# Kernel optimization log

Measured on AMD Instinct MI355X. Metric: run time of the kernel, lower is better.

The kernel has to match this reference:

```python
import jax, jax.numpy as jnp
import numpy as np


def setup_inputs() -> dict:
    key = jax.random.key(0)
    ks = jax.random.split(key, 8)
    B, L, F, H, A = 128, 196, 2048, 512, 512
    features = jax.random.normal(ks[0], (B, L, F), dtype=jnp.float32)
    hidden_state = jax.random.normal(ks[1], (B, H), dtype=jnp.float32)
    # Linear params (PyTorch layout: weight [out, in], bias [out]); scaled like kaiming-uniform
    W_enc = jax.random.normal(ks[2], (A, F), dtype=jnp.float32) / np.sqrt(F)
    b_enc = jnp.zeros((A,), dtype=jnp.float32)
    W_dec = jax.random.normal(ks[3], (A, H), dtype=jnp.float32) / np.sqrt(H)
    b_dec = jnp.zeros((A,), dtype=jnp.float32)
    W_com = jax.random.normal(ks[4], (1, A), dtype=jnp.float32) / np.sqrt(A)
    b_com = jnp.zeros((1,), dtype=jnp.float32)
    return {
        "features": features, "hidden_state": hidden_state,
        "W_enc": W_enc, "b_enc": b_enc,
        "W_dec": W_dec, "b_dec": b_dec,
        "W_com": W_com, "b_com": b_com,
    }


def reference(features, hidden_state, W_enc, b_enc, W_dec, b_dec, W_com, b_com):
    # encoder_context: [B, L, A]
    enc = jnp.einsum('blf,af->bla', features, W_enc) + b_enc
    # decoder_context: [B, 1, A]
    dec = (hidden_state @ W_dec.T + b_dec)[:, None, :]
    # relu + linear to scalar score (dropout in eval mode = identity): [B, L]
    scores = jnp.einsum('bla,a->bl', jax.nn.relu(enc + dec), W_com[0]) + b_com[0]
    alpha = jax.nn.softmax(scores, axis=1)  # [B, L]
    weighted_features = jnp.einsum('blf,bl->bf', features, alpha)  # [B, F]
    return weighted_features, alpha
```

## Files before the change

### kernel.cpp

```cpp
#include <hip/hip_runtime.h>
#include <hip/hip_bf16.h>
#include <math.h>

#define B_  128
#define L_  196
#define F_  2048
#define H_  512
#define A_  512
#define ML_ (B_*L_)

typedef _Float16 half8 __attribute__((ext_vector_type(8)));
typedef _Float16 half4v __attribute__((ext_vector_type(4)));
typedef float f32x4 __attribute__((ext_vector_type(4)));

__device__ __forceinline__ void gld_lds16(const void* g, void* l) {
  __builtin_amdgcn_global_load_lds((const __attribute__((address_space(1))) void*)g,
                                   (__attribute__((address_space(3))) void*)l, 16, 0, 0);
}

__global__ __launch_bounds__(256) void k_prep(const float4* __restrict__ Wenc4,
                                              half4v* __restrict__ wH,
                                              const float* __restrict__ hs,
                                              const float* __restrict__ Wdec,
                                              const float* __restrict__ bdec,
                                              const float* __restrict__ benc,
                                              float* __restrict__ dec,
                                              float* __restrict__ scores) {
  const int b = blockIdx.x, t = threadIdx.x;

  {
    const int base = b * 2048 + t;
    float4 v[8];
#pragma unroll
    for (int j = 0; j < 8; j++) v[j] = Wenc4[base + j * 256];
#pragma unroll
    for (int j = 0; j < 8; j++) {
      half4v o = { (_Float16)v[j].x, (_Float16)v[j].y, (_Float16)v[j].z, (_Float16)v[j].w };
      wH[base + j * 256] = o;
    }
  }

  const int g = b * 256 + t;
  if (g < ML_) scores[g] = 0.f;

  __shared__ float h[H_];
  h[t]       = hs[b * H_ + t];
  h[t + 256] = hs[b * H_ + t + 256];
  __syncthreads();

#pragma unroll
  for (int r = 0; r < 2; r++) {
    const int a = t + r * 256;
    float acc = bdec[a] + benc[a];
    const float4* wr = (const float4*)(Wdec + (size_t)a * H_);
#pragma unroll 4
    for (int k4 = 0; k4 < H_ / 4; k4++) {
      const float4 w = wr[k4];
      acc += w.x * h[4*k4] + w.y * h[4*k4+1] + w.z * h[4*k4+2] + w.w * h[4*k4+3];
    }
    dec[b * A_ + a] = acc;
  }
}

__global__ __launch_bounds__(256) void k_scores_mfma(const float* __restrict__ fA,
                                                     const _Float16* __restrict__ fB,
                                                     const float* __restrict__ dec,
                                                     const float* __restrict__ wcom,
                                                     float* __restrict__ scores) {
  __shared__ float     As[128 * 64];
  __shared__ _Float16  Bs[128 * 64];
  __shared__ float decS[2][128];

  const int tid  = threadIdx.x;
  const int lane = tid & 63;
  const int w    = tid >> 6;
  const int a0   = blockIdx.x * 128;
  const int m0   = blockIdx.y * 128;
  const int wm   = w & 1;
  const int wn   = w >> 1;
  const int quad = lane >> 4;
  const int l16  = lane & 15;

  f32x4 acc[4][4];
#pragma unroll
  for (int i = 0; i < 4; i++)
#pragma unroll
    for (int j = 0; j < 4; j++)
#pragma unroll
      for (int k = 0; k < 4; k++) acc[i][j][k] = 0.f;

  const int b0 = m0 / L_;
  {
    const int i = tid >> 7;
    const int j = tid & 127;
    int bb = b0 + i; if (bb > B_ - 1) bb = B_ - 1;
    decS[i][j] = dec[bb * A_ + a0 + j];
  }

  const int srow4  = lane >> 4;
  const int slot16 = lane & 15;
  const float* pA[8];
#pragma unroll
  for (int i = 0; i < 8; i++) {
    const int rb = w * 32 + i * 4;
    const int r  = rb + srow4;
    const int ch = slot16 ^ (r & 15);
    pA[i] = fA + (size_t)(m0 + r) * F_ + ch * 4;
  }
  const int srow8 = lane >> 3;
  const int slot8 = lane & 7;
  const _Float16* pB[4];
#pragma unroll
  for (int i = 0; i < 4; i++) {
    const int rb = w * 32 + i * 8;
    const int r  = rb + srow8;
    const int ch = slot8 ^ (r & 7);
    pB[i] = fB + (size_t)(a0 + r) * F_ + ch * 8;
  }

  for (int kt = 0; kt < F_; kt += 64) {
#pragma unroll
    for (int i = 0; i < 8; i++)
      gld_lds16(pA[i] + kt, &As[(w * 32 + i * 4) * 64]);
#pragma unroll
    for (int i = 0; i < 4; i++)
      gld_lds16(pB[i] + kt, &Bs[(w * 32 + i * 8) * 64]);
    __syncthreads();

#pragma unroll
    for (int k32 = 0; k32 < 2; k32++) {
      half8 af[4], bf[4];
#pragma unroll
      for (int mt = 0; mt < 4; mt++) {
        const int row = wm * 64 + mt * 16 + l16;
        const int g   = k32 * 8 + quad * 2;
        const float4 f0 = *(const float4*)&As[row * 64 + ((g    ) ^ l16) * 4];
        const float4 f1 = *(const float4*)&As[row * 64 + ((g + 1) ^ l16) * 4];
        half8 a;
        a[0] = (_Float16)f0.x; a[1] = (_Float16)f0.y;
        a[2] = (_Float16)f0.z; a[3] = (_Float16)f0.w;
        a[4] = (_Float16)f1.x; a[5] = (_Float16)f1.y;
        a[6] = (_Float16)f1.z; a[7] = (_Float16)f1.w;
        af[mt] = a;
      }
#pragma unroll
      for (int at = 0; at < 4; at++) {
        const int row = wn * 64 + at * 16 + l16;
        const int pos = (k32 * 4 + quad) ^ (row & 7);
        bf[at] = *(const half8*)&Bs[row * 64 + pos * 8];
      }
#pragma unroll
      for (int mt = 0; mt < 4; mt++)
#pragma unroll
        for (int at = 0; at < 4; at++)
          acc[mt][at] = __builtin_amdgcn_mfma_f32_16x16x32_f16(af[mt], bf[at], acc[mt][at], 0, 0, 0);
    }
    __syncthreads();
  }

  float w4[4];
#pragma unroll
  for (int at = 0; at < 4; at++) w4[at] = wcom[a0 + wn * 64 + at * 16 + l16];

#pragma unroll
  for (int mt = 0; mt < 4; mt++) {
#pragma unroll
    for (int r = 0; r < 4; r++) {
      const int m  = m0 + wm * 64 + mt * 16 + quad * 4 + r;
      const int db = m / L_ - b0;
      float p = 0.f;
#pragma unroll
      for (int at = 0; at < 4; at++) {
        const float e = acc[mt][at][r] + decS[db][wn * 64 + at * 16 + l16];
        p = fmaf(fmaxf(e, 0.f), w4[at], p);
      }
      p += __shfl_xor(p, 1);
      p += __shfl_xor(p, 2);
      p += __shfl_xor(p, 4);
      p += __shfl_xor(p, 8);
      if (l16 == 0) atomicAdd(&scores[m], p);
    }
  }
}

__global__ __launch_bounds__(256) void k_attn_f32(const float* __restrict__ feat,
                                                  const float* __restrict__ scores,
                                                  float* __restrict__ alpha,
                                                  float* __restrict__ out) {
  const int fc = blockIdx.x, b = blockIdx.y, t = threadIdx.x;
  __shared__ float al[L_];
  __shared__ float redm[4];
  __shared__ float reds[4];

  float s = (t < L_) ? scores[b * L_ + t] : -INFINITY;
  float m = s;
#pragma unroll
  for (int o = 32; o >= 1; o >>= 1) m = fmaxf(m, __shfl_xor(m, o));
  if ((t & 63) == 0) redm[t >> 6] = m;
  __syncthreads();
  m = fmaxf(fmaxf(redm[0], redm[1]), fmaxf(redm[2], redm[3]));
  float e = (t < L_) ? expf(s - m) : 0.f;
  float sum = e;
#pragma unroll
  for (int o = 32; o >= 1; o >>= 1) sum += __shfl_xor(sum, o);
  if ((t & 63) == 0) reds[t >> 6] = sum;
  __syncthreads();
  sum = reds[0] + reds[1] + reds[2] + reds[3];
  if (t < L_) {
    const float a = e / sum;
    al[t] = a;
    if (fc == 0) alpha[b * L_ + t] = a;
  }
  __syncthreads();

  const int f0 = fc * 512 + t * 2;
  const float2* fp = (const float2*)(feat + (size_t)b * L_ * F_ + f0);
  float ax = 0.f, ay = 0.f;
#pragma unroll 4
  for (int l = 0; l < L_; l++) {
    const float2 v = fp[(size_t)l * (F_ / 2)];
    const float wgt = al[l];
    ax = fmaf(v.x, wgt, ax);
    ay = fmaf(v.y, wgt, ay);
  }
  float2 o = { ax, ay };
  *(float2*)(out + (size_t)b * F_ + f0) = o;
}

__global__ __launch_bounds__(256) void k_scores_f32(const float* __restrict__ feat,
                                                    const float* __restrict__ Wenc,
                                                    const float* __restrict__ dec,
                                                    const float* __restrict__ wcom,
                                                    float* __restrict__ scores) {
  __shared__ float As[16][128];
  __shared__ float Bs[16][128];
  const int tid = threadIdx.x;
  const int m0 = blockIdx.x * 128;
  const int a0 = blockIdx.y * 128;
  const int tx = tid & 15;
  const int ty = tid >> 4;
  float acc[8][8];
#pragma unroll
  for (int i = 0; i < 8; i++)
#pragma unroll
    for (int j = 0; j < 8; j++) acc[i][j] = 0.f;
  for (int kt = 0; kt < F_; kt += 16) {
#pragma unroll
    for (int rep = 0; rep < 2; rep++) {
      const int idx = rep * 256 + tid;
      const int row = idx >> 2;
      const int kp  = (idx & 3) << 2;
      const float4 v = *(const float4*)(feat + (size_t)(m0 + row) * F_ + kt + kp);
      As[kp+0][row] = v.x; As[kp+1][row] = v.y; As[kp+2][row] = v.z; As[kp+3][row] = v.w;
      const float4 w = *(const float4*)(Wenc + (size_t)(a0 + row) * F_ + kt + kp);
      Bs[kp+0][row] = w.x; Bs[kp+1][row] = w.y; Bs[kp+2][row] = w.z; Bs[kp+3][row] = w.w;
    }
    __syncthreads();
#pragma unroll
    for (int k = 0; k < 16; k++) {
      float ar[8], br[8];
      *(float4*)&ar[0] = *(const float4*)&As[k][ty * 8];
      *(float4*)&ar[4] = *(const float4*)&As[k][ty * 8 + 4];
      *(float4*)&br[0] = *(const float4*)&Bs[k][tx * 8];
      *(float4*)&br[4] = *(const float4*)&Bs[k][tx * 8 + 4];
#pragma unroll
      for (int i = 0; i < 8; i++)
#pragma unroll
        for (int j = 0; j < 8; j++) acc[i][j] = fmaf(ar[i], br[j], acc[i][j]);
    }
    __syncthreads();
  }
  float w8[8];
  *(float4*)&w8[0] = *(const float4*)(wcom + a0 + tx * 8);
  *(float4*)&w8[4] = *(const float4*)(wcom + a0 + tx * 8 + 4);
#pragma unroll
  for (int i = 0; i < 8; i++) {
    const int m = m0 + ty * 8 + i;
    const int b = m / L_;
    const float* dp = dec + b * A_ + a0 + tx * 8;
    float p = 0.f;
#pragma unroll
    for (int j = 0; j < 8; j++) {
      const float e = acc[i][j] + dp[j];
      p = fmaf(fmaxf(e, 0.f), w8[j], p);
    }
    p += __shfl_xor(p, 1);
    p += __shfl_xor(p, 2);
    p += __shfl_xor(p, 4);
    p += __shfl_xor(p, 8);
    if (tx == 0) atomicAdd(&scores[m], p);
  }
}

__global__ __launch_bounds__(256) void k_dec_only(const float* __restrict__ hs,
                                                  const float* __restrict__ Wdec,
                                                  const float* __restrict__ bdec,
                                                  const float* __restrict__ benc,
                                                  float* __restrict__ dec,
                                                  float* __restrict__ scores) {
  const int b = blockIdx.x, t = threadIdx.x;
  const int g = b * 256 + t;
  if (g < ML_) scores[g] = 0.f;
  __shared__ float h[H_];
  h[t]       = hs[b * H_ + t];
  h[t + 256] = hs[b * H_ + t + 256];
  __syncthreads();
#pragma unroll
  for (int r = 0; r < 2; r++) {
    const int a = t + r * 256;
    float acc = bdec[a] + benc[a];
    const float4* wr = (const float4*)(Wdec + (size_t)a * H_);
#pragma unroll 4
    for (int k4 = 0; k4 < H_ / 4; k4++) {
      const float4 w = wr[k4];
      acc += w.x * h[4*k4] + w.y * h[4*k4+1] + w.z * h[4*k4+2] + w.w * h[4*k4+3];
    }
    dec[b * A_ + a] = acc;
  }
}

extern "C" void kernel_launch(void* const* d_in, const int* in_sizes, int n_in,
                              void* d_out, int out_size, void* d_ws, size_t ws_size,
                              hipStream_t stream) {
  const float* feat = (const float*)d_in[0];
  const float* hs   = (const float*)d_in[1];
  const float* Wenc = (const float*)d_in[2];
  const float* benc = (const float*)d_in[3];
  const float* Wdec = (const float*)d_in[4];
  const float* bdec = (const float*)d_in[5];
  const float* wcom = (const float*)d_in[6];

  float* out   = (float*)d_out;
  float* alpha = out + B_ * F_;
  float* dec    = (float*)d_ws;
  float* scores = dec + B_ * A_;

  const size_t need = (size_t)(B_ * A_ + ML_) * 4 + (size_t)A_ * F_ * 2;

  if (ws_size >= need) {
    _Float16* wH = (_Float16*)(scores + ML_);
    k_prep<<<dim3(128), dim3(256), 0, stream>>>(
        (const float4*)Wenc, (half4v*)wH, hs, Wdec, bdec, benc, dec, scores);
    k_scores_mfma<<<dim3(A_ / 128, ML_ / 128), dim3(256), 0, stream>>>(feat, wH, dec, wcom, scores);
  } else {
    k_dec_only<<<dim3(B_), dim3(256), 0, stream>>>(hs, Wdec, bdec, benc, dec, scores);
    k_scores_f32<<<dim3(ML_ / 128, A_ / 128), dim3(256), 0, stream>>>(feat, Wenc, dec, wcom, scores);
  }
  k_attn_f32<<<dim3(4, B_), dim3(256), 0, stream>>>(feat, scores, alpha, out);
}
```

Before: 500.2 us.

## Halve K-tile, add occupancy hint and grouped block ordering in scores MFMA kernel

```diff
diff --git a/kernel.cpp b/kernel.cpp
--- a/kernel.cpp
+++ b/kernel.cpp
@@ -62,20 +62,26 @@
   }
 }
 
-__global__ __launch_bounds__(256) void k_scores_mfma(const float* __restrict__ fA,
-                                                     const _Float16* __restrict__ fB,
-                                                     const float* __restrict__ dec,
-                                                     const float* __restrict__ wcom,
-                                                     float* __restrict__ scores) {
-  __shared__ float     As[128 * 64];
-  __shared__ _Float16  Bs[128 * 64];
+__global__ __launch_bounds__(256, 5) void k_scores_mfma(const float* __restrict__ fA,
+                                                        const _Float16* __restrict__ fB,
+                                                        const float* __restrict__ dec,
+                                                        const float* __restrict__ wcom,
+                                                        float* __restrict__ scores) {
+  __shared__ float     As[128 * 32];
+  __shared__ _Float16  Bs[128 * 32];
   __shared__ float decS[2][128];
 
   const int tid  = threadIdx.x;
   const int lane = tid & 63;
   const int w    = tid >> 6;
-  const int a0   = blockIdx.x * 128;
-  const int m0   = blockIdx.y * 128;
+
+  const int l = blockIdx.x;
+  int at_, mt;
+  if (l < 768) { at_ = (l >> 3) & 3; mt = (l >> 5) * 8 + (l & 7); }
+  else { const int idx = l - 768; at_ = idx >> 2; mt = 192 + (idx & 3); }
+  const int a0 = at_ * 128;
+  const int m0 = mt * 128;
+
   const int wm   = w & 1;
   const int wn   = w >> 1;
   const int quad = lane >> 4;
@@ -97,64 +103,58 @@
     decS[i][j] = dec[bb * A_ + a0 + j];
   }
 
-  const int srow4  = lane >> 4;
-  const int slot16 = lane & 15;
-  const float* pA[8];
-#pragma unroll
-  for (int i = 0; i < 8; i++) {
-    const int rb = w * 32 + i * 4;
-    const int r  = rb + srow4;
-    const int ch = slot16 ^ (r & 15);
-    pA[i] = fA + (size_t)(m0 + r) * F_ + ch * 4;
-  }
-  const int srow8 = lane >> 3;
-  const int slot8 = lane & 7;
-  const _Float16* pB[4];
+  const int srowA = lane >> 3;
+  const int gA    = (lane & 7) ^ srowA;
+  const float* pA[4];
 #pragma unroll
   for (int i = 0; i < 4; i++) {
     const int rb = w * 32 + i * 8;
-    const int r  = rb + srow8;
-    const int ch = slot8 ^ (r & 7);
-    pB[i] = fB + (size_t)(a0 + r) * F_ + ch * 8;
-  }
-
-  for (int kt = 0; kt < F_; kt += 64) {
-#pragma unroll
-    for (int i = 0; i < 8; i++)
-      gld_lds16(pA[i] + kt, &As[(w * 32 + i * 4) * 64]);
+    pA[i] = fA + (size_t)(m0 + rb + srowA) * F_ + gA * 4;
+  }
+  const int srowB = lane >> 2;
+  const int gB    = (lane & 3) ^ (srowB & 3);
+  const _Float16* pB[2];
+#pragma unroll
+  for (int i = 0; i < 2; i++) {
+    const int rb = w * 32 + i * 16;
+    pB[i] = fB + (size_t)(a0 + rb + srowB) * F_ + gB * 8;
+  }
+
+  for (int kt = 0; kt < F_; kt += 32) {
 #pragma unroll
     for (int i = 0; i < 4; i++)
-      gld_lds16(pB[i] + kt, &Bs[(w * 32 + i * 8) * 64]);
+      gld_lds16(pA[i] + kt, &As[(w * 32 + i * 8) * 32]);
+#pragma unroll
+    for (int i = 0; i < 2; i++)
+      gld_lds16(pB[i] + kt, &Bs[(w * 32 + i * 16) * 32]);
     __syncthreads();
 
-#pragma unroll
-    for (int k32 = 0; k32 < 2; k32++) {
-      half8 af[4], bf[4];
-#pragma unroll
-      for (int mt = 0; mt < 4; mt++) {
-        const int row = wm * 64 + mt * 16 + l16;
-        const int g   = k32 * 8 + quad * 2;
-        const float4 f0 = *(const float4*)&As[row * 64 + ((g    ) ^ l16) * 4];
-        const float4 f1 = *(const float4*)&As[row * 64 + ((g + 1) ^ l16) * 4];
-        half8 a;
-        a[0] = (_Float16)f0.x; a[1] = (_Float16)f0.y;
-        a[2] = (_Float16)f0.z; a[3] = (_Float16)f0.w;
-        a[4] = (_Float16)f1.x; a[5] = (_Float16)f1.y;
-        a[6] = (_Float16)f1.z; a[7] = (_Float16)f1.w;
-        af[mt] = a;
-      }
-#pragma unroll
-      for (int at = 0; at < 4; at++) {
-        const int row = wn * 64 + at * 16 + l16;
-        const int pos = (k32 * 4 + quad) ^ (row & 7);
-        bf[at] = *(const half8*)&Bs[row * 64 + pos * 8];
-      }
-#pragma unroll
-      for (int mt = 0; mt < 4; mt++)
-#pragma unroll
-        for (int at = 0; at < 4; at++)
-          acc[mt][at] = __builtin_amdgcn_mfma_f32_16x16x32_f16(af[mt], bf[at], acc[mt][at], 0, 0, 0);
-    }
+    half8 af[4], bf[4];
+#pragma unroll
+    for (int mf = 0; mf < 4; mf++) {
+      const int row = wm * 64 + mf * 16 + l16;
+      const int s0  = (quad * 2) ^ (row & 7);
+      const int s1  = s0 ^ 1;
+      const float4 f0 = *(const float4*)&As[row * 32 + s0 * 4];
+      const float4 f1 = *(const float4*)&As[row * 32 + s1 * 4];
+      half8 a;
+      a[0] = (_Float16)f0.x; a[1] = (_Float16)f0.y;
+      a[2] = (_Float16)f0.z; a[3] = (_Float16)f0.w;
+      a[4] = (_Float16)f1.x; a[5] = (_Float16)f1.y;
+      a[6] = (_Float16)f1.z; a[7] = (_Float16)f1.w;
+      af[mf] = a;
+    }
+#pragma unroll
+    for (int at = 0; at < 4; at++) {
+      const int row = wn * 64 + at * 16 + l16;
+      const int pos = quad ^ (row & 3);
+      bf[at] = *(const half8*)&Bs[row * 32 + pos * 8];
+    }
+#pragma unroll
+    for (int mf = 0; mf < 4; mf++)
+#pragma unroll
+      for (int at = 0; at < 4; at++)
+        acc[mf][at] = __builtin_amdgcn_mfma_f32_16x16x32_f16(af[mf], bf[at], acc[mf][at], 0, 0, 0);
     __syncthreads();
   }
 
@@ -163,15 +163,15 @@
   for (int at = 0; at < 4; at++) w4[at] = wcom[a0 + wn * 64 + at * 16 + l16];
 
 #pragma unroll
-  for (int mt = 0; mt < 4; mt++) {
+  for (int mf = 0; mf < 4; mf++) {
 #pragma unroll
     for (int r = 0; r < 4; r++) {
-      const int m  = m0 + wm * 64 + mt * 16 + quad * 4 + r;
+      const int m  = m0 + wm * 64 + mf * 16 + quad * 4 + r;
       const int db = m / L_ - b0;
       float p = 0.f;
 #pragma unroll
       for (int at = 0; at < 4; at++) {
-        const float e = acc[mt][at][r] + decS[db][wn * 64 + at * 16 + l16];
+        const float e = acc[mf][at][r] + decS[db][wn * 64 + at * 16 + l16];
         p = fmaf(fmaxf(e, 0.f), w4[at], p);
       }
       p += __shfl_xor(p, 1);
@@ -217,9 +217,9 @@
   const float2* fp = (const float2*)(feat + (size_t)b * L_ * F_ + f0);
   float ax = 0.f, ay = 0.f;
 #pragma unroll 4
-  for (int l = 0; l < L_; l++) {
-    const float2 v = fp[(size_t)l * (F_ / 2)];
-    const float wgt = al[l];
+  for (int ll = 0; ll < L_; ll++) {
+    const float2 v = fp[(size_t)ll * (F_ / 2)];
+    const float wgt = al[ll];
     ax = fmaf(v.x, wgt, ax);
     ay = fmaf(v.y, wgt, ay);
   }
@@ -341,7 +341,7 @@
     _Float16* wH = (_Float16*)(scores + ML_);
     k_prep<<<dim3(128), dim3(256), 0, stream>>>(
         (const float4*)Wenc, (half4v*)wH, hs, Wdec, bdec, benc, dec, scores);
-    k_scores_mfma<<<dim3(A_ / 128, ML_ / 128), dim3(256), 0, stream>>>(feat, wH, dec, wcom, scores);
+    k_scores_mfma<<<dim3(784), dim3(256), 0, stream>>>(feat, wH, dec, wcom, scores);
   } else {
     k_dec_only<<<dim3(B_), dim3(256), 0, stream>>>(hs, Wdec, bdec, benc, dec, scores);
     k_scores_f32<<<dim3(ML_ / 128, A_ / 128), dim3(256), 0, stream>>>(feat, Wenc, dec, wcom, scores);
```

New measurement: 602.3 us. 1.2x slower.
